# Kernel optimization log

Hardware: AMD Instinct MI355X
Metric: run time of the kernel (lower is better)

Reference implementation:

```python
import jax, jax.numpy as jnp
import numpy as np

# Qwen3-MoE style config
B, S, D = 2, 2048, 2048        # batch, seqlen, hidden_size
E, I, TOPK = 64, 768, 8        # num_experts, moe_intermediate_size, num_experts_per_tok
M = B * S                      # tokens
CAP = 2 * (M * TOPK) // E


def setup_inputs() -> dict:
    key = jax.random.key(0)
    k0, k1, k2, k3, k4 = jax.random.split(key, 5)
    return {
        "x": jax.random.normal(k0, (B, S, D), jnp.float32),
        "router_weight": jax.random.normal(k1, (D, E), jnp.float32) * 0.02,
        "gate_proj": jax.random.normal(k2, (E, D, I), jnp.float32) * 0.02,
        "up_proj": jax.random.normal(k3, (E, D, I), jnp.float32) * 0.02,
        "down_proj": jax.random.normal(k4, (E, I, D), jnp.float32) * 0.02,
    }


def _moe(x, router_weight, gate_proj, up_proj, down_proj):
    b, s, d = x.shape
    xf = x.reshape(-1, d)                                  # [M, d]
    m = xf.shape[0]

    # ---- TokenChoiceTopKRouter: softmax scores, top-k, renormalize ----
    logits = xf @ router_weight                            # [M, E]
    probs = jax.nn.softmax(logits.astype(jnp.float32), axis=-1)
    topw, topi = jax.lax.top_k(probs, TOPK)                # [M, k]
    topw = topw / topw.sum(axis=-1, keepdims=True)         # norm_topk_prob

    flat_e = topi.reshape(-1)                              # [M*k] expert id per assignment
    flat_w = topw.reshape(-1).astype(x.dtype)              # [M*k] routing weight per assignment

    # ---- permute: sort assignments by expert (stable) ----
    order = jnp.argsort(flat_e)                            # [M*k]
    se = flat_e[order]                                     # sorted expert ids
    tok = order // TOPK                                    # source token per sorted assignment
    counts = jax.ops.segment_sum(jnp.ones_like(flat_e), flat_e, num_segments=E)
    starts = jnp.cumsum(counts) - counts                   # exclusive prefix sum
    pos = jnp.arange(m * TOPK) - starts[se]                # slot within expert's buffer
    valid = pos < CAP
    posc = jnp.minimum(pos, CAP - 1)

    # ---- dispatch to padded per-expert buffers [E, CAP, d] ----
    xe = jnp.zeros((E, CAP, d), x.dtype).at[se, pos].set(xf[tok], mode='drop')

    # ---- grouped SwiGLU experts (batched GEMMs) ----
    h = jax.nn.silu(jnp.einsum('ecd,edi->eci', xe, gate_proj)) \
        * jnp.einsum('ecd,edi->eci', xe, up_proj)          # [E, CAP, I]
    ye = jnp.einsum('eci,eid->ecd', h, down_proj)          # [E, CAP, d]

    # ---- unpermute + weighted combine ----
    contrib = jnp.where(valid[:, None], ye[se, posc], 0.0) * flat_w[order][:, None]
    out = jnp.zeros((m, d), x.dtype).at[tok].add(contrib)  # sum over topk per token
    return out.reshape(b, s, d)


def reference(x, router_weight, gate_proj, up_proj, down_proj):
    return _moe(x, router_weight, gate_proj, up_proj, down_proj)
```

## Files before the change

### kernel.cpp

```cpp
#include <hip/hip_runtime.h>
#include <hip/hip_bf16.h>

typedef __attribute__((ext_vector_type(4))) float f32x4;
typedef __attribute__((ext_vector_type(8))) short bf16x8;
typedef __attribute__((ext_vector_type(8))) unsigned short us8;
typedef unsigned int   u32;
typedef unsigned short u16;

#define D_DIM 2048
#define I_DIM 768
#define NE    64
#define CAP   1024
#define NTOK  4096

__device__ __forceinline__ u32 cvt2(float a, float b) {
  __hip_bfloat162 hh = __float22bfloat162_rn(float2{a, b});
  union { __hip_bfloat162 h; u32 u; } c; c.h = hh; return c.u;
}
__device__ __forceinline__ u16 f2b(float f) {
  __hip_bfloat16 b = __float2bfloat16(f);
  union { __hip_bfloat16 b; u16 u; } c; c.b = b; return c.u;
}
__device__ __forceinline__ float b2f(u16 v) {
  union { u32 u; float f; } c; c.u = (u32)v << 16; return c.f;
}
__device__ __forceinline__ void glp16(const void* g, void* l) {
  __builtin_amdgcn_global_load_lds(
      (const __attribute__((address_space(1))) u32*)g,
      (__attribute__((address_space(3))) u32*)l, 16, 0, 0);
}

#define VMW(n) asm volatile("s_waitcnt vmcnt(" #n ")" ::: "memory")
#define BARF   do { __builtin_amdgcn_s_barrier(); \
                    asm volatile("" ::: "memory"); } while (0)

__global__ __launch_bounds__(256) void k_cvt_x(const float* __restrict__ x,
                                               u16* __restrict__ xb) {
  const size_t i = ((size_t)blockIdx.x * 256 + threadIdx.x) * 8;
  float4 v0 = *(const float4*)(x + i);
  float4 v1 = *(const float4*)(x + i + 4);
  uint4 o;
  o.x = cvt2(v0.x, v0.y); o.y = cvt2(v0.z, v0.w);
  o.z = cvt2(v1.x, v1.y); o.w = cvt2(v1.z, v1.w);
  *(uint4*)(xb + i) = o;
}

__global__ __launch_bounds__(256) void k_router(
    const float* __restrict__ x, const float* __restrict__ rw,
    int* __restrict__ counts, int* __restrict__ slot_token,
    float* __restrict__ slot_w)
{
  const int lane = threadIdx.x & 63;
  const int tok  = blockIdx.x * 4 + (threadIdx.x >> 6);
  const float* xr = x + (size_t)tok * D_DIM;

  float acc = 0.f;
  for (int d0 = 0; d0 < D_DIM; d0 += 64) {
    float xv = xr[d0 + lane];
    #pragma unroll
    for (int j = 0; j < 64; ++j) {
      float xj = __shfl(xv, j, 64);
      acc = fmaf(xj, rw[(size_t)(d0 + j) * NE + lane], acc);
    }
  }

  float v = acc; int vi = lane;
  float wk[8]; int ei[8];
  float mx0 = 0.f, wsum = 0.f;
  #pragma unroll
  for (int k = 0; k < 8; ++k) {
    float mv = v; int mi = vi;
    #pragma unroll
    for (int off = 32; off >= 1; off >>= 1) {
      float ov = __shfl_xor(mv, off, 64);
      int   oi = __shfl_xor(mi, off, 64);
      if (ov > mv || (ov == mv && oi < mi)) { mv = ov; mi = oi; }
    }
    if (k == 0) mx0 = mv;
    float ew = __expf(mv - mx0);
    wk[k] = ew; ei[k] = mi; wsum += ew;
    if (lane == mi) v = -3.4e38f;
  }

  if (lane == 0) {
    float inv = 1.f / wsum;
    #pragma unroll
    for (int k = 0; k < 8; ++k) {
      int ee   = ei[k];
      int slot = atomicAdd(&counts[ee], 1);
      if (slot < CAP) {
        slot_token[ee * CAP + slot] = tok;
        slot_w[ee * CAP + slot]     = wk[k] * inv;
      }
    }
  }
}

__global__ __launch_bounds__(256) void k_inv(
    const int* __restrict__ counts, const int* __restrict__ slot_token,
    int* __restrict__ tok_cnt, int* __restrict__ tok_idx)
{
  const int e = blockIdx.x;
  int cnt = counts[e]; if (cnt > CAP) cnt = CAP;
  for (int s = threadIdx.x; s < cnt; s += 256) {
    const int tok = slot_token[e * CAP + s];
    const int pos = atomicAdd(&tok_cnt[tok], 1);
    if (pos < 8) tok_idx[tok * 8 + pos] = e * CAP + s;
  }
}

__global__ __launch_bounds__(256) void k_wpack(const float* __restrict__ in,
                                               u16* __restrict__ outp,
                                               int R, int C) {
  const int e  = blockIdx.z;
  const int c0 = blockIdx.x * 64;
  const int r0 = blockIdx.y * 64;
  const float* ip = in + (size_t)e * R * C;
  u16* op = outp + (size_t)e * (size_t)(C / 64) * (R / 8) * 512
                 + ((size_t)(c0 / 64) * (R / 8) + (r0 / 8)) * 512;

  __shared__ u16 T[64][76];
  const int t  = threadIdx.x;
  const int rr = t >> 4;
  const int cc = (t & 15) * 4;
  #pragma unroll
  for (int it = 0; it < 4; ++it) {
    const int r = rr + it * 16;
    float4 v = *(const float4*)(ip + (size_t)(r0 + r) * C + c0 + cc);
    T[cc + 0][r] = f2b(v.x);
    T[cc + 1][r] = f2b(v.y);
    T[cc + 2][r] = f2b(v.z);
    T[cc + 3][r] = f2b(v.w);
  }
  __syncthreads();
  const int n = t & 63;
  #pragma unroll
  for (int p = 0; p < 2; ++p) {
    const int c = (t >> 6) + p * 4;
    const u16* s = &T[n][c * 8];
    uint4 o;
    o.x = (u32)s[0] | ((u32)s[1] << 16);
    o.y = (u32)s[2] | ((u32)s[3] << 16);
    o.z = (u32)s[4] | ((u32)s[5] << 16);
    o.w = (u32)s[6] | ((u32)s[7] << 16);
    *(uint4*)(op + ((size_t)c * 64 + n) * 8) = o;
  }
}

__global__ __launch_bounds__(256) void k_xpack(
    const u16* __restrict__ xb, const int* __restrict__ counts,
    const int* __restrict__ slot_token, u16* __restrict__ xeT)
{
  const int e   = blockIdx.z;
  const int s0  = blockIdx.y * 64;
  const int kc0 = blockIdx.x * 32;
  int cnt = counts[e]; if (cnt > CAP) cnt = CAP;

  __shared__ u16 T[64][264];
  const int t = threadIdx.x;
  const int r = t >> 2;
  const int q = t & 3;
  const int  tok  = slot_token[e * CAP + s0 + r];
  const bool live = (s0 + r) < cnt;
  const u16* src = xb + (size_t)tok * D_DIM + kc0 * 8;

  #pragma unroll
  for (int it = 0; it < 8; ++it) {
    const int kl = it * 32 + q * 8;
    us8 v = {0, 0, 0, 0, 0, 0, 0, 0};
    if (live) v = *(const us8*)(src + kl);
    *(us8*)&T[r][kl] = v;
  }
  __syncthreads();

  u16* dst = xeT + (size_t)e * 2097152 + (size_t)kc0 * 8192 + (size_t)s0 * 8;
  const int sl = t & 63;
  #pragma unroll
  for (int p = 0; p < 8; ++p) {
    const int c = (t >> 6) + p * 4;
    const u16* s = &T[sl][c * 8];
    uint4 o = *(const uint4*)s;
    *(uint4*)(dst + (size_t)c * 8192 + sl * 8) = o;
  }
}


__device__ __forceinline__ void m1_issue(
    const u16* xeA, const u16* gbp, const u16* ubp, u16* sm,
    int js, int sb, int wv, int lane, int m0)
{
  const int st = sb * 16384;
  if (wv < 4) {
    const u16* s = xeA + (size_t)(js * 4) * 8192 + (size_t)(m0 + wv * 64 + lane) * 8;
    u16* d = sm + st + (wv * 64) * 8;
    glp16(s,         d);
    glp16(s + 8192,  d + 2048);
    glp16(s + 16384, d + 4096);
    glp16(s + 24576, d + 6144);
  } else {
    const int w2 = wv & 1;
    const u16* base = (wv >= 6) ? ubp : gbp;
    const u16* s = base + (size_t)w2 * 131072 + (size_t)(js * 4) * 512 + lane * 8;
    u16* d = sm + st + ((wv >= 6) ? 12288 : 8192) + (w2 * 64) * 8;
    glp16(s,        d);
    glp16(s + 512,  d + 1024);
    glp16(s + 1024, d + 2048);
    glp16(s + 1536, d + 3072);
  }
}

__device__ __forceinline__ void m1_step(
    const u16* sm, int st, int gq, int li, int mrow, int icol,
    f32x4 (&ag)[4][4], f32x4 (&au)[4][4])
{
  bf16x8 a[4], g[4], u[4];
  #pragma unroll
  for (int mf = 0; mf < 4; ++mf)
    a[mf] = *(const bf16x8*)&sm[st + (gq * 256 + mrow + mf * 16 + li) * 8];
  #pragma unroll
  for (int nf = 0; nf < 4; ++nf) {
    g[nf] = *(const bf16x8*)&sm[st + 8192  + (gq * 128 + icol + nf * 16 + li) * 8];
    u[nf] = *(const bf16x8*)&sm[st + 12288 + (gq * 128 + icol + nf * 16 + li) * 8];
  }
  #pragma unroll
  for (int mf = 0; mf < 4; ++mf)
    #pragma unroll
    for (int nf = 0; nf < 4; ++nf) {
      ag[mf][nf] = __builtin_amdgcn_mfma_f32_16x16x32_bf16(a[mf], g[nf], ag[mf][nf], 0, 0, 0);
      au[mf][nf] = __builtin_amdgcn_mfma_f32_16x16x32_bf16(a[mf], u[nf], au[mf][nf], 0, 0, 0);
    }
}

__global__ __launch_bounds__(512, 2) void k_mlp1p(
    const u16* __restrict__ xeT, const u16* __restrict__ Gpk,
    const u16* __restrict__ Upk, const int* __restrict__ counts,
    u16* __restrict__ hP)
{
  extern __shared__ u16 sm[];
  const int i   = blockIdx.x;
  const int xcd = i & 7;
  const int p   = i >> 3;
  const int mt  = p & 3;
  const int pe  = p >> 2;
  const int val = pe * 8 + xcd;
  const int e   = val / 6;
  const int nt  = val % 6;

  int cnt = counts[e]; if (cnt > CAP) cnt = CAP;
  const int m0 = mt * 256;
  if (m0 >= cnt) return;

  const int t = threadIdx.x;
  const int lane = t & 63, wv = t >> 6;
  const int li = lane & 15, gq = lane >> 4;
  const int mrow = (wv >> 1) * 64, icol = (wv & 1) * 64;

  const u16* xeA = xeT + (size_t)e * 2097152;
  const u16* gbp = Gpk + (size_t)e * 1572864 + (size_t)(nt * 2) * 131072;
  const u16* ubp = Upk + (size_t)e * 1572864 + (size_t)(nt * 2) * 131072;

  f32x4 ag[4][4], au[4][4];
  #pragma unroll
  for (int mf = 0; mf < 4; ++mf)
    #pragma unroll
    for (int nf = 0; nf < 4; ++nf) {
      f32x4 z = {0.f, 0.f, 0.f, 0.f};
      ag[mf][nf] = z; au[mf][nf] = z;
    }

  m1_issue(xeA, gbp, ubp, sm, 0, 0, wv, lane, m0);
  m1_issue(xeA, gbp, ubp, sm, 1, 1, wv, lane, m0);
  m1_issue(xeA, gbp, ubp, sm, 2, 2, wv, lane, m0);

  for (int j = 0; j < 61; ++j) {
    VMW(8); BARF;
    m1_issue(xeA, gbp, ubp, sm, j + 3, (j + 3) & 3, wv, lane, m0);
    m1_step(sm, (j & 3) * 16384, gq, li, mrow, icol, ag, au);
  }
  VMW(8); BARF; m1_step(sm, 1 * 16384, gq, li, mrow, icol, ag, au);
  VMW(4); BARF; m1_step(sm, 2 * 16384, gq, li, mrow, icol, ag, au);
  VMW(0); BARF; m1_step(sm, 3 * 16384, gq, li, mrow, icol, ag, au);

  u16* hPe = hP + (size_t)e * 786432;
  #pragma unroll
  for (int mf = 0; mf < 4; ++mf)
    #pragma unroll
    for (int jj = 0; jj < 4; ++jj) {
      const int slot = m0 + mrow + mf * 16 + gq * 4 + jj;
      #pragma unroll
      for (int nf = 0; nf < 4; ++nf) {
        const int ii = nt * 128 + icol + nf * 16 + li;
        float gg = ag[mf][nf][jj];
        float uu = au[mf][nf][jj];
        hPe[(size_t)(ii >> 3) * 8192 + slot * 8 + (ii & 7)] =
            f2b(gg * uu / (1.f + __expf(-gg)));
      }
    }
}

__device__ __forceinline__ void m2_issue(
    const u16* hPe, const u16* dpe, u16* sm,
    int js, int sb, int wv, int lane, int m0)
{
  const int st = sb * 16384;
  if (wv < 4) {
    const u16* s = hPe + (size_t)(js * 4) * 8192 + (size_t)(m0 + wv * 64 + lane) * 8;
    u16* d = sm + st + (wv * 64) * 8;
    glp16(s,         d);
    glp16(s + 8192,  d + 2048);
    glp16(s + 16384, d + 4096);
    glp16(s + 24576, d + 6144);
  } else {
    const int w2 = wv - 4;
    const u16* s = dpe + (size_t)w2 * 49152 + (size_t)(js * 4) * 512 + lane * 8;
    u16* d = sm + st + 8192 + (w2 * 64) * 8;
    glp16(s,        d);
    glp16(s + 512,  d + 2048);
    glp16(s + 1024, d + 4096);
    glp16(s + 1536, d + 6144);
  }
}

__device__ __forceinline__ void m2_step(
    const u16* sm, int st, int gq, int li, int mrow, int ncol,
    f32x4 (&acc)[4][8])
{
  bf16x8 a[4], b[8];
  #pragma unroll
  for (int mf = 0; mf < 4; ++mf)
    a[mf] = *(const bf16x8*)&sm[st + (gq * 256 + mrow + mf * 16 + li) * 8];
  #pragma unroll
  for (int nf = 0; nf < 8; ++nf)
    b[nf] = *(const bf16x8*)&sm[st + 8192 + (gq * 256 + ncol + nf * 16 + li) * 8];
  #pragma unroll
  for (int mf = 0; mf < 4; ++mf)
    #pragma unroll
    for (int nf = 0; nf < 8; ++nf)
      acc[mf][nf] = __builtin_amdgcn_mfma_f32_16x16x32_bf16(a[mf], b[nf], acc[mf][nf], 0, 0, 0);
}

__global__ __launch_bounds__(512, 2) void k_mlp2p(
    const u16* __restrict__ hP, const u16* __restrict__ Dpk,
    const int* __restrict__ counts, const float* __restrict__ slot_w,
    u16* __restrict__ ye)
{
  extern __shared__ u16 sm[];
  const int i   = blockIdx.x;
  const int xcd = i & 7;
  const int p   = i >> 3;
  const int mt  = p & 3;
  const int pe  = p >> 2;
  const int val = pe * 8 + xcd;
  const int e   = val >> 3;
  const int nt  = val & 7;

  int cnt = counts[e]; if (cnt > CAP) cnt = CAP;
  const int m0 = mt * 256;
  if (m0 >= cnt) return;
  const int n0 = nt * 256;

  const int t = threadIdx.x;
  const int lane = t & 63, wv = t >> 6;
  const int li = lane & 15, gq = lane >> 4;
  const int mrow = (wv >> 1) * 64, ncol = (wv & 1) * 128;

  const u16* hPe = hP + (size_t)e * 786432;
  const u16* dpe = Dpk + (size_t)e * 1572864 + (size_t)(nt * 4) * 49152;

  f32x4 acc[4][8];
  #pragma unroll
  for (int mf = 0; mf < 4; ++mf)
    #pragma unroll
    for (int nf = 0; nf < 8; ++nf) { f32x4 z = {0.f,0.f,0.f,0.f}; acc[mf][nf] = z; }

  m2_issue(hPe, dpe, sm, 0, 0, wv, lane, m0);
  m2_issue(hPe, dpe, sm, 1, 1, wv, lane, m0);
  m2_issue(hPe, dpe, sm, 2, 2, wv, lane, m0);

  for (int j = 0; j < 21; ++j) {
    VMW(8); BARF;
    m2_issue(hPe, dpe, sm, j + 3, (j + 3) & 3, wv, lane, m0);
    m2_step(sm, (j & 3) * 16384, gq, li, mrow, ncol, acc);
  }
  VMW(8); BARF; m2_step(sm, 1 * 16384, gq, li, mrow, ncol, acc);
  VMW(4); BARF; m2_step(sm, 2 * 16384, gq, li, mrow, ncol, acc);
  VMW(0); BARF; m2_step(sm, 3 * 16384, gq, li, mrow, ncol, acc);

  #pragma unroll
  for (int mf = 0; mf < 4; ++mf)
    #pragma unroll
    for (int jj = 0; jj < 4; ++jj) {
      const int slot = m0 + mrow + mf * 16 + gq * 4 + jj;
      if (slot < cnt) {
        const float wgt = slot_w[e * CAP + slot];
        u16* yr = ye + (size_t)(e * CAP + slot) * D_DIM + n0 + ncol + li;
        #pragma unroll
        for (int nf = 0; nf < 8; ++nf)
          yr[nf * 16] = f2b(wgt * acc[mf][nf][jj]);
      }
    }
}

__global__ __launch_bounds__(256) void k_combine(
    const u16* __restrict__ ye, const int* __restrict__ tok_idx,
    const int* __restrict__ tok_cnt, float* __restrict__ out)
{
  const int tok = blockIdx.x;
  const int c0  = threadIdx.x * 8;
  int cnt8 = tok_cnt[tok]; if (cnt8 > 8) cnt8 = 8;

  float s[8] = {0.f, 0.f, 0.f, 0.f, 0.f, 0.f, 0.f, 0.f};
  #pragma unroll
  for (int k = 0; k < 8; ++k) {
    if (k < cnt8) {
      const int idx = tok_idx[tok * 8 + k];
      const us8 v = *(const us8*)(ye + (size_t)idx * D_DIM + c0);
      #pragma unroll
      for (int j = 0; j < 8; ++j) s[j] += b2f(v[j]);
    }
  }
  float4 o0 = {s[0], s[1], s[2], s[3]};
  float4 o1 = {s[4], s[5], s[6], s[7]};
  float* op = out + (size_t)tok * D_DIM + c0;
  *(float4*)op       = o0;
  *(float4*)(op + 4) = o1;
}

extern "C" void kernel_launch(void* const* d_in, const int* in_sizes, int n_in,
                              void* d_out, int out_size, void* d_ws, size_t ws_size,
                              hipStream_t stream) {
  const float* x    = (const float*)d_in[0];
  const float* rw   = (const float*)d_in[1];
  const float* gate = (const float*)d_in[2];
  const float* up   = (const float*)d_in[3];
  const float* down = (const float*)d_in[4];
  float* out = (float*)d_out;

  char* ws = (char*)d_ws;
  int*   counts     = (int*)ws;
  int*   slot_token = (int*)(ws + 1024);
  float* slot_w     = (float*)(ws + 263168);
  u16*   xb         = (u16*)(ws + 525312);
  u16*   hP         = (u16*)(ws + 17302528);
  u16*   Gpk        = (u16*)(ws + 117965824);
  u16*   Upk        = (u16*)(ws + 319292416);
  u16*   xeT        = (u16*)(ws + 520619008);
  u16*   Dpk        = xeT;
  u16*   ye         = Gpk;
  int*   tok_cnt    = (int*)(ws + 721945600);
  int*   tok_idx    = (int*)(ws + 721945600 + 16384);

  hipFuncSetAttribute((const void*)k_mlp1p,
                      hipFuncAttributeMaxDynamicSharedMemorySize, 131072);
  hipFuncSetAttribute((const void*)k_mlp2p,
                      hipFuncAttributeMaxDynamicSharedMemorySize, 131072);

  hipMemsetAsync(counts, 0, NE * sizeof(int), stream);
  hipMemsetAsync(slot_token, 0, (size_t)NE * CAP * sizeof(int), stream);

  k_cvt_x <<<dim3((NTOK * D_DIM) / (256 * 8)), 256, 0, stream>>>(x, xb);
  k_router<<<dim3(NTOK / 4),                   256, 0, stream>>>(x, rw, counts, slot_token, slot_w);

  k_wpack<<<dim3(12, 32, NE), 256, 0, stream>>>(gate, Gpk, D_DIM, I_DIM);
  k_wpack<<<dim3(12, 32, NE), 256, 0, stream>>>(up,   Upk, D_DIM, I_DIM);
  k_xpack<<<dim3(8, 16, NE),  256, 0, stream>>>(xb, counts, slot_token, xeT);
  k_mlp1p<<<dim3(1536), 512, 131072, stream>>>(xeT, Gpk, Upk, counts, hP);

  hipMemsetAsync(tok_cnt, 0, NTOK * sizeof(int), stream);
  k_inv  <<<dim3(NE), 256, 0, stream>>>(counts, slot_token, tok_cnt, tok_idx);
  k_wpack<<<dim3(32, 12, NE), 256, 0, stream>>>(down, Dpk, I_DIM, D_DIM);

  k_mlp2p  <<<dim3(2048), 512, 131072, stream>>>(hP, Dpk, counts, slot_w, ye);
  k_combine<<<dim3(NTOK), 256, 0, stream>>>(ye, tok_idx, tok_cnt, out);
}
```

Before: 1.249 ms.

## Make expert GEMM blocks loop over all live M-tiles with continuous prefetch pipeline

Each workgroup in both expert GEMM kernels now owns one (expert, N-tile) pair and walks every live 256-row M tile of that expert in sequence. The global-to-LDS prefetch pipeline runs straight across tile boundaries, with an epilogue and accumulator reset at each tile end. This removes the per-block pipeline warm-up and drain and the launch of idle blocks for empty M tiles. The cost is far fewer workgroups (384 and 512 instead of 1536 and 2048), which risks lower occupancy and load imbalance, since experts with more tokens run longer.

```diff
diff --git a/kernel.cpp b/kernel.cpp
--- a/kernel.cpp
+++ b/kernel.cpp
@@ -187,11 +187,11 @@
 
 __device__ __forceinline__ void m1_issue(
     const u16* xeA, const u16* gbp, const u16* ubp, u16* sm,
-    int js, int sb, int wv, int lane, int m0)
+    int js, int sb, int wv, int lane, int sm0)
 {
   const int st = sb * 16384;
   if (wv < 4) {
-    const u16* s = xeA + (size_t)(js * 4) * 8192 + (size_t)(m0 + wv * 64 + lane) * 8;
+    const u16* s = xeA + (size_t)(js * 4) * 8192 + (size_t)(sm0 + wv * 64 + lane) * 8;
     u16* d = sm + st + (wv * 64) * 8;
     glp16(s,         d);
     glp16(s + 8192,  d + 2048);
@@ -231,57 +231,10 @@
     }
 }
 
-__global__ __launch_bounds__(512, 2) void k_mlp1p(
-    const u16* __restrict__ xeT, const u16* __restrict__ Gpk,
-    const u16* __restrict__ Upk, const int* __restrict__ counts,
-    u16* __restrict__ hP)
-{
-  extern __shared__ u16 sm[];
-  const int i   = blockIdx.x;
-  const int xcd = i & 7;
-  const int p   = i >> 3;
-  const int mt  = p & 3;
-  const int pe  = p >> 2;
-  const int val = pe * 8 + xcd;
-  const int e   = val / 6;
-  const int nt  = val % 6;
-
-  int cnt = counts[e]; if (cnt > CAP) cnt = CAP;
-  const int m0 = mt * 256;
-  if (m0 >= cnt) return;
-
-  const int t = threadIdx.x;
-  const int lane = t & 63, wv = t >> 6;
-  const int li = lane & 15, gq = lane >> 4;
-  const int mrow = (wv >> 1) * 64, icol = (wv & 1) * 64;
-
-  const u16* xeA = xeT + (size_t)e * 2097152;
-  const u16* gbp = Gpk + (size_t)e * 1572864 + (size_t)(nt * 2) * 131072;
-  const u16* ubp = Upk + (size_t)e * 1572864 + (size_t)(nt * 2) * 131072;
-
-  f32x4 ag[4][4], au[4][4];
-  #pragma unroll
-  for (int mf = 0; mf < 4; ++mf)
-    #pragma unroll
-    for (int nf = 0; nf < 4; ++nf) {
-      f32x4 z = {0.f, 0.f, 0.f, 0.f};
-      ag[mf][nf] = z; au[mf][nf] = z;
-    }
-
-  m1_issue(xeA, gbp, ubp, sm, 0, 0, wv, lane, m0);
-  m1_issue(xeA, gbp, ubp, sm, 1, 1, wv, lane, m0);
-  m1_issue(xeA, gbp, ubp, sm, 2, 2, wv, lane, m0);
-
-  for (int j = 0; j < 61; ++j) {
-    VMW(8); BARF;
-    m1_issue(xeA, gbp, ubp, sm, j + 3, (j + 3) & 3, wv, lane, m0);
-    m1_step(sm, (j & 3) * 16384, gq, li, mrow, icol, ag, au);
-  }
-  VMW(8); BARF; m1_step(sm, 1 * 16384, gq, li, mrow, icol, ag, au);
-  VMW(4); BARF; m1_step(sm, 2 * 16384, gq, li, mrow, icol, ag, au);
-  VMW(0); BARF; m1_step(sm, 3 * 16384, gq, li, mrow, icol, ag, au);
-
-  u16* hPe = hP + (size_t)e * 786432;
+__device__ __forceinline__ void m1_epi(
+    u16* hPe, int nt, int m0, int mrow, int icol, int gq, int li,
+    f32x4 (&ag)[4][4], f32x4 (&au)[4][4])
+{
   #pragma unroll
   for (int mf = 0; mf < 4; ++mf)
     #pragma unroll
@@ -296,15 +249,80 @@
             f2b(gg * uu / (1.f + __expf(-gg)));
       }
     }
+  #pragma unroll
+  for (int mf = 0; mf < 4; ++mf)
+    #pragma unroll
+    for (int nf = 0; nf < 4; ++nf) {
+      f32x4 z = {0.f, 0.f, 0.f, 0.f};
+      ag[mf][nf] = z; au[mf][nf] = z;
+    }
+}
+
+__global__ __launch_bounds__(512, 2) void k_mlp1p(
+    const u16* __restrict__ xeT, const u16* __restrict__ Gpk,
+    const u16* __restrict__ Upk, const int* __restrict__ counts,
+    u16* __restrict__ hP)
+{
+  extern __shared__ u16 sm[];
+  const int i   = blockIdx.x;
+  const int xcd = i & 7;
+  const int p   = i >> 3;
+  const int val = p * 8 + xcd;
+  const int e   = val / 6;
+  const int nt  = val % 6;
+
+  int cnt = counts[e]; if (cnt > CAP) cnt = CAP;
+  if (cnt <= 0) return;
+  const int nlive = (cnt + 255) >> 8;
+  const int NT = nlive * 64;
+
+  const int t = threadIdx.x;
+  const int lane = t & 63, wv = t >> 6;
+  const int li = lane & 15, gq = lane >> 4;
+  const int mrow = (wv >> 1) * 64, icol = (wv & 1) * 64;
+
+  const u16* xeA = xeT + (size_t)e * 2097152;
+  const u16* gbp = Gpk + (size_t)e * 1572864 + (size_t)(nt * 2) * 131072;
+  const u16* ubp = Upk + (size_t)e * 1572864 + (size_t)(nt * 2) * 131072;
+  u16* hPe = hP + (size_t)e * 786432;
+
+  f32x4 ag[4][4], au[4][4];
+  #pragma unroll
+  for (int mf = 0; mf < 4; ++mf)
+    #pragma unroll
+    for (int nf = 0; nf < 4; ++nf) {
+      f32x4 z = {0.f, 0.f, 0.f, 0.f};
+      ag[mf][nf] = z; au[mf][nf] = z;
+    }
+
+  m1_issue(xeA, gbp, ubp, sm, 0, 0, wv, lane, 0);
+  m1_issue(xeA, gbp, ubp, sm, 1, 1, wv, lane, 0);
+  m1_issue(xeA, gbp, ubp, sm, 2, 2, wv, lane, 0);
+
+  for (int jj = 0; jj < NT - 3; ++jj) {
+    VMW(8); BARF;
+    const int s = jj + 3;
+    m1_issue(xeA, gbp, ubp, sm, s & 63, s & 3, wv, lane, (s >> 6) * 256);
+    m1_step(sm, (jj & 3) * 16384, gq, li, mrow, icol, ag, au);
+    if ((jj & 63) == 63)
+      m1_epi(hPe, nt, (jj >> 6) * 256, mrow, icol, gq, li, ag, au);
+  }
+  { const int jj = NT - 3; VMW(8); BARF;
+    m1_step(sm, (jj & 3) * 16384, gq, li, mrow, icol, ag, au); }
+  { const int jj = NT - 2; VMW(4); BARF;
+    m1_step(sm, (jj & 3) * 16384, gq, li, mrow, icol, ag, au); }
+  { const int jj = NT - 1; VMW(0); BARF;
+    m1_step(sm, (jj & 3) * 16384, gq, li, mrow, icol, ag, au);
+    m1_epi(hPe, nt, (jj >> 6) * 256, mrow, icol, gq, li, ag, au); }
 }
 
 __device__ __forceinline__ void m2_issue(
     const u16* hPe, const u16* dpe, u16* sm,
-    int js, int sb, int wv, int lane, int m0)
+    int ph, int sb, int wv, int lane, int sm0)
 {
   const int st = sb * 16384;
   if (wv < 4) {
-    const u16* s = hPe + (size_t)(js * 4) * 8192 + (size_t)(m0 + wv * 64 + lane) * 8;
+    const u16* s = hPe + (size_t)(ph * 4) * 8192 + (size_t)(sm0 + wv * 64 + lane) * 8;
     u16* d = sm + st + (wv * 64) * 8;
     glp16(s,         d);
     glp16(s + 8192,  d + 2048);
@@ -312,7 +330,7 @@
     glp16(s + 24576, d + 6144);
   } else {
     const int w2 = wv - 4;
-    const u16* s = dpe + (size_t)w2 * 49152 + (size_t)(js * 4) * 512 + lane * 8;
+    const u16* s = dpe + (size_t)w2 * 49152 + (size_t)(ph * 4) * 512 + lane * 8;
     u16* d = sm + st + 8192 + (w2 * 64) * 8;
     glp16(s,        d);
     glp16(s + 512,  d + 2048);
@@ -339,6 +357,29 @@
       acc[mf][nf] = __builtin_amdgcn_mfma_f32_16x16x32_bf16(a[mf], b[nf], acc[mf][nf], 0, 0, 0);
 }
 
+__device__ __forceinline__ void m2_epi(
+    u16* ye, int cnt, const float* slot_w, int eCAP, int n0, int m0,
+    int mrow, int ncol, int gq, int li, f32x4 (&acc)[4][8])
+{
+  #pragma unroll
+  for (int mf = 0; mf < 4; ++mf)
+    #pragma unroll
+    for (int jj = 0; jj < 4; ++jj) {
+      const int slot = m0 + mrow + mf * 16 + gq * 4 + jj;
+      if (slot < cnt) {
+        const float wgt = slot_w[eCAP + slot];
+        u16* yr = ye + (size_t)(eCAP + slot) * D_DIM + n0 + ncol + li;
+        #pragma unroll
+        for (int nf = 0; nf < 8; ++nf)
+          yr[nf * 16] = f2b(wgt * acc[mf][nf][jj]);
+      }
+    }
+  #pragma unroll
+  for (int mf = 0; mf < 4; ++mf)
+    #pragma unroll
+    for (int nf = 0; nf < 8; ++nf) { f32x4 z = {0.f,0.f,0.f,0.f}; acc[mf][nf] = z; }
+}
+
 __global__ __launch_bounds__(512, 2) void k_mlp2p(
     const u16* __restrict__ hP, const u16* __restrict__ Dpk,
     const int* __restrict__ counts, const float* __restrict__ slot_w,
@@ -348,15 +389,14 @@
   const int i   = blockIdx.x;
   const int xcd = i & 7;
   const int p   = i >> 3;
-  const int mt  = p & 3;
-  const int pe  = p >> 2;
-  const int val = pe * 8 + xcd;
+  const int val = p * 8 + xcd;
   const int e   = val >> 3;
   const int nt  = val & 7;
 
   int cnt = counts[e]; if (cnt > CAP) cnt = CAP;
-  const int m0 = mt * 256;
-  if (m0 >= cnt) return;
+  if (cnt <= 0) return;
+  const int nlive = (cnt + 255) >> 8;
+  const int NT = nlive * 24;
   const int n0 = nt * 256;
 
   const int t = threadIdx.x;
@@ -366,6 +406,7 @@
 
   const u16* hPe = hP + (size_t)e * 786432;
   const u16* dpe = Dpk + (size_t)e * 1572864 + (size_t)(nt * 4) * 49152;
+  const int eCAP = e * CAP;
 
   f32x4 acc[4][8];
   #pragma unroll
@@ -373,32 +414,27 @@
     #pragma unroll
     for (int nf = 0; nf < 8; ++nf) { f32x4 z = {0.f,0.f,0.f,0.f}; acc[mf][nf] = z; }
 
-  m2_issue(hPe, dpe, sm, 0, 0, wv, lane, m0);
-  m2_issue(hPe, dpe, sm, 1, 1, wv, lane, m0);
-  m2_issue(hPe, dpe, sm, 2, 2, wv, lane, m0);
-
-  for (int j = 0; j < 21; ++j) {
+  m2_issue(hPe, dpe, sm, 0, 0, wv, lane, 0);
+  m2_issue(hPe, dpe, sm, 1, 1, wv, lane, 0);
+  m2_issue(hPe, dpe, sm, 2, 2, wv, lane, 0);
+
+  for (int jj = 0; jj < NT - 3; ++jj) {
     VMW(8); BARF;
-    m2_issue(hPe, dpe, sm, j + 3, (j + 3) & 3, wv, lane, m0);
-    m2_step(sm, (j & 3) * 16384, gq, li, mrow, ncol, acc);
-  }
-  VMW(8); BARF; m2_step(sm, 1 * 16384, gq, li, mrow, ncol, acc);
-  VMW(4); BARF; m2_step(sm, 2 * 16384, gq, li, mrow, ncol, acc);
-  VMW(0); BARF; m2_step(sm, 3 * 16384, gq, li, mrow, ncol, acc);
-
-  #pragma unroll
-  for (int mf = 0; mf < 4; ++mf)
-    #pragma unroll
-    for (int jj = 0; jj < 4; ++jj) {
-      const int slot = m0 + mrow + mf * 16 + gq * 4 + jj;
-      if (slot < cnt) {
-        const float wgt = slot_w[e * CAP + slot];
-        u16* yr = ye + (size_t)(e * CAP + slot) * D_DIM + n0 + ncol + li;
-        #pragma unroll
-        for (int nf = 0; nf < 8; ++nf)
-          yr[nf * 16] = f2b(wgt * acc[mf][nf][jj]);
-      }
-    }
+    const int s    = jj + 3;
+    const int tixs = (s >= 72) ? 3 : (s >= 48) ? 2 : (s >= 24) ? 1 : 0;
+    m2_issue(hPe, dpe, sm, s - tixs * 24, s & 3, wv, lane, tixs * 256);
+    m2_step(sm, (jj & 3) * 16384, gq, li, mrow, ncol, acc);
+    const int tixj = (jj >= 72) ? 3 : (jj >= 48) ? 2 : (jj >= 24) ? 1 : 0;
+    if (jj - tixj * 24 == 23)
+      m2_epi(ye, cnt, slot_w, eCAP, n0, tixj * 256, mrow, ncol, gq, li, acc);
+  }
+  { const int jj = NT - 3; VMW(8); BARF;
+    m2_step(sm, (jj & 3) * 16384, gq, li, mrow, ncol, acc); }
+  { const int jj = NT - 2; VMW(4); BARF;
+    m2_step(sm, (jj & 3) * 16384, gq, li, mrow, ncol, acc); }
+  { const int jj = NT - 1; VMW(0); BARF;
+    m2_step(sm, (jj & 3) * 16384, gq, li, mrow, ncol, acc);
+    m2_epi(ye, cnt, slot_w, eCAP, n0, (nlive - 1) * 256, mrow, ncol, gq, li, acc); }
 }
 
 __global__ __launch_bounds__(256) void k_combine(
@@ -464,12 +500,12 @@
   k_wpack<<<dim3(12, 32, NE), 256, 0, stream>>>(gate, Gpk, D_DIM, I_DIM);
   k_wpack<<<dim3(12, 32, NE), 256, 0, stream>>>(up,   Upk, D_DIM, I_DIM);
   k_xpack<<<dim3(8, 16, NE),  256, 0, stream>>>(xb, counts, slot_token, xeT);
-  k_mlp1p<<<dim3(1536), 512, 131072, stream>>>(xeT, Gpk, Upk, counts, hP);
+  k_mlp1p<<<dim3(384), 512, 131072, stream>>>(xeT, Gpk, Upk, counts, hP);
 
   hipMemsetAsync(tok_cnt, 0, NTOK * sizeof(int), stream);
   k_inv  <<<dim3(NE), 256, 0, stream>>>(counts, slot_token, tok_cnt, tok_idx);
   k_wpack<<<dim3(32, 12, NE), 256, 0, stream>>>(down, Dpk, I_DIM, D_DIM);
 
-  k_mlp2p  <<<dim3(2048), 512, 131072, stream>>>(hP, Dpk, counts, slot_w, ye);
+  k_mlp2p  <<<dim3(512), 512, 131072, stream>>>(hP, Dpk, counts, slot_w, ye);
   k_combine<<<dim3(NTOK), 256, 0, stream>>>(ye, tok_idx, tok_cnt, out);
 }
```

Measured after the change: 1.310 ms. +4.9%, slower.

## Halve grouped-GEMM M tile to 128 with 256-thread blocks and triple-buffered LDS

Applied to the files above, without the earlier changes.

Both expert GEMM kernels move from 256-row tiles with 512 threads and a 4-stage LDS ring to 128-row tiles with 256 threads and a 3-stage ring. Each block now uses 72 KB of shared memory instead of 128 KB, and the grids double. The load-issue code is rewritten so 4 waves cover A and B tile loads. The aim is finer granularity, so experts with fewer tokens waste less padded work and more blocks fit per CU. In exchange, the B weight tiles are read twice as often per expert, and the pipeline is one stage shallower.

```diff
diff --git a/kernel.cpp b/kernel.cpp
--- a/kernel.cpp
+++ b/kernel.cpp
@@ -186,41 +186,40 @@
 
 
 __device__ __forceinline__ void m1_issue(
-    const u16* xeA, const u16* gbp, const u16* ubp, u16* sm,
-    int js, int sb, int wv, int lane, int m0)
-{
-  const int st = sb * 16384;
-  if (wv < 4) {
-    const u16* s = xeA + (size_t)(js * 4) * 8192 + (size_t)(m0 + wv * 64 + lane) * 8;
-    u16* d = sm + st + (wv * 64) * 8;
-    glp16(s,         d);
-    glp16(s + 8192,  d + 2048);
-    glp16(s + 16384, d + 4096);
-    glp16(s + 24576, d + 6144);
-  } else {
-    const int w2 = wv & 1;
-    const u16* base = (wv >= 6) ? ubp : gbp;
-    const u16* s = base + (size_t)w2 * 131072 + (size_t)(js * 4) * 512 + lane * 8;
-    u16* d = sm + st + ((wv >= 6) ? 12288 : 8192) + (w2 * 64) * 8;
-    glp16(s,        d);
-    glp16(s + 512,  d + 1024);
-    glp16(s + 1024, d + 2048);
-    glp16(s + 1536, d + 3072);
+    const u16* xeA, const u16* gb, const u16* ub, u16* st,
+    int js, int wv, int lane, int m0)
+{
+  #pragma unroll
+  for (int q = 0; q < 6; ++q) {
+    const int id = wv * 6 + q;
+    const int kc = (id >> 1) & 3;
+    const int h  = id & 1;
+    const size_t kcA = (size_t)(js * 4 + kc);
+    if (id < 8) {
+      glp16(xeA + kcA * 8192 + (size_t)(m0 + h * 64 + lane) * 8,
+            st + kc * 1024 + h * 512);
+    } else if (id < 16) {
+      glp16(gb + (size_t)h * 131072 + kcA * 512 + lane * 8,
+            st + 4096 + kc * 1024 + h * 512);
+    } else {
+      glp16(ub + (size_t)h * 131072 + kcA * 512 + lane * 8,
+            st + 8192 + kc * 1024 + h * 512);
+    }
   }
 }
 
 __device__ __forceinline__ void m1_step(
-    const u16* sm, int st, int gq, int li, int mrow, int icol,
+    const u16* st, int gq, int li, int mrow, int icol,
     f32x4 (&ag)[4][4], f32x4 (&au)[4][4])
 {
   bf16x8 a[4], g[4], u[4];
   #pragma unroll
   for (int mf = 0; mf < 4; ++mf)
-    a[mf] = *(const bf16x8*)&sm[st + (gq * 256 + mrow + mf * 16 + li) * 8];
+    a[mf] = *(const bf16x8*)&st[(gq * 128 + mrow + mf * 16 + li) * 8];
   #pragma unroll
   for (int nf = 0; nf < 4; ++nf) {
-    g[nf] = *(const bf16x8*)&sm[st + 8192  + (gq * 128 + icol + nf * 16 + li) * 8];
-    u[nf] = *(const bf16x8*)&sm[st + 12288 + (gq * 128 + icol + nf * 16 + li) * 8];
+    g[nf] = *(const bf16x8*)&st[4096 + (gq * 128 + icol + nf * 16 + li) * 8];
+    u[nf] = *(const bf16x8*)&st[8192 + (gq * 128 + icol + nf * 16 + li) * 8];
   }
   #pragma unroll
   for (int mf = 0; mf < 4; ++mf)
@@ -231,7 +230,7 @@
     }
 }
 
-__global__ __launch_bounds__(512, 2) void k_mlp1p(
+__global__ __launch_bounds__(256, 2) void k_mlp1p(
     const u16* __restrict__ xeT, const u16* __restrict__ Gpk,
     const u16* __restrict__ Upk, const int* __restrict__ counts,
     u16* __restrict__ hP)
@@ -240,14 +239,14 @@
   const int i   = blockIdx.x;
   const int xcd = i & 7;
   const int p   = i >> 3;
-  const int mt  = p & 3;
-  const int pe  = p >> 2;
+  const int mt  = p & 7;
+  const int pe  = p >> 3;
   const int val = pe * 8 + xcd;
   const int e   = val / 6;
   const int nt  = val % 6;
 
   int cnt = counts[e]; if (cnt > CAP) cnt = CAP;
-  const int m0 = mt * 256;
+  const int m0 = mt * 128;
   if (m0 >= cnt) return;
 
   const int t = threadIdx.x;
@@ -256,8 +255,9 @@
   const int mrow = (wv >> 1) * 64, icol = (wv & 1) * 64;
 
   const u16* xeA = xeT + (size_t)e * 2097152;
-  const u16* gbp = Gpk + (size_t)e * 1572864 + (size_t)(nt * 2) * 131072;
-  const u16* ubp = Upk + (size_t)e * 1572864 + (size_t)(nt * 2) * 131072;
+  const u16* gb  = Gpk + (size_t)e * 1572864 + (size_t)(nt * 2) * 131072;
+  const u16* ub  = Upk + (size_t)e * 1572864 + (size_t)(nt * 2) * 131072;
+  u16* hPe = hP + (size_t)e * 786432;
 
   f32x4 ag[4][4], au[4][4];
   #pragma unroll
@@ -268,20 +268,17 @@
       ag[mf][nf] = z; au[mf][nf] = z;
     }
 
-  m1_issue(xeA, gbp, ubp, sm, 0, 0, wv, lane, m0);
-  m1_issue(xeA, gbp, ubp, sm, 1, 1, wv, lane, m0);
-  m1_issue(xeA, gbp, ubp, sm, 2, 2, wv, lane, m0);
-
-  for (int j = 0; j < 61; ++j) {
-    VMW(8); BARF;
-    m1_issue(xeA, gbp, ubp, sm, j + 3, (j + 3) & 3, wv, lane, m0);
-    m1_step(sm, (j & 3) * 16384, gq, li, mrow, icol, ag, au);
-  }
-  VMW(8); BARF; m1_step(sm, 1 * 16384, gq, li, mrow, icol, ag, au);
-  VMW(4); BARF; m1_step(sm, 2 * 16384, gq, li, mrow, icol, ag, au);
-  VMW(0); BARF; m1_step(sm, 3 * 16384, gq, li, mrow, icol, ag, au);
-
-  u16* hPe = hP + (size_t)e * 786432;
+  m1_issue(xeA, gb, ub, sm,         0, wv, lane, m0);
+  m1_issue(xeA, gb, ub, sm + 12288, 1, wv, lane, m0);
+
+  for (int j = 0; j < 62; ++j) {
+    VMW(6); BARF;
+    m1_issue(xeA, gb, ub, sm + ((j + 2) % 3) * 12288, j + 2, wv, lane, m0);
+    m1_step(sm + (j % 3) * 12288, gq, li, mrow, icol, ag, au);
+  }
+  VMW(6); BARF; m1_step(sm + 2 * 12288, gq, li, mrow, icol, ag, au);
+  VMW(0); BARF; m1_step(sm + 0 * 12288, gq, li, mrow, icol, ag, au);
+
   #pragma unroll
   for (int mf = 0; mf < 4; ++mf)
     #pragma unroll
@@ -299,39 +296,39 @@
 }
 
 __device__ __forceinline__ void m2_issue(
-    const u16* hPe, const u16* dpe, u16* sm,
-    int js, int sb, int wv, int lane, int m0)
-{
-  const int st = sb * 16384;
-  if (wv < 4) {
-    const u16* s = hPe + (size_t)(js * 4) * 8192 + (size_t)(m0 + wv * 64 + lane) * 8;
-    u16* d = sm + st + (wv * 64) * 8;
-    glp16(s,         d);
-    glp16(s + 8192,  d + 2048);
-    glp16(s + 16384, d + 4096);
-    glp16(s + 24576, d + 6144);
-  } else {
-    const int w2 = wv - 4;
-    const u16* s = dpe + (size_t)w2 * 49152 + (size_t)(js * 4) * 512 + lane * 8;
-    u16* d = sm + st + 8192 + (w2 * 64) * 8;
-    glp16(s,        d);
-    glp16(s + 512,  d + 2048);
-    glp16(s + 1024, d + 4096);
-    glp16(s + 1536, d + 6144);
+    const u16* hPe, const u16* dp, u16* st,
+    int js, int wv, int lane, int m0)
+{
+  #pragma unroll
+  for (int q = 0; q < 6; ++q) {
+    const int id = wv * 6 + q;
+    const size_t kcA = (size_t)(js * 4 + ((id < 8) ? ((id >> 1) & 3) : ((id - 8) & 3)));
+    if (id < 8) {
+      const int kc = (id >> 1) & 3;
+      const int h  = id & 1;
+      glp16(hPe + kcA * 8192 + (size_t)(m0 + h * 64 + lane) * 8,
+            st + kc * 1024 + h * 512);
+    } else {
+      const int r  = id - 8;
+      const int kc = r & 3;
+      const int ng = r >> 2;
+      glp16(dp + (size_t)ng * 49152 + kcA * 512 + lane * 8,
+            st + 4096 + kc * 2048 + ng * 512);
+    }
   }
 }
 
 __device__ __forceinline__ void m2_step(
-    const u16* sm, int st, int gq, int li, int mrow, int ncol,
+    const u16* st, int gq, int li, int mrow, int ncol,
     f32x4 (&acc)[4][8])
 {
   bf16x8 a[4], b[8];
   #pragma unroll
   for (int mf = 0; mf < 4; ++mf)
-    a[mf] = *(const bf16x8*)&sm[st + (gq * 256 + mrow + mf * 16 + li) * 8];
+    a[mf] = *(const bf16x8*)&st[(gq * 128 + mrow + mf * 16 + li) * 8];
   #pragma unroll
   for (int nf = 0; nf < 8; ++nf)
-    b[nf] = *(const bf16x8*)&sm[st + 8192 + (gq * 256 + ncol + nf * 16 + li) * 8];
+    b[nf] = *(const bf16x8*)&st[4096 + (gq * 256 + ncol + nf * 16 + li) * 8];
   #pragma unroll
   for (int mf = 0; mf < 4; ++mf)
     #pragma unroll
@@ -339,7 +336,7 @@
       acc[mf][nf] = __builtin_amdgcn_mfma_f32_16x16x32_bf16(a[mf], b[nf], acc[mf][nf], 0, 0, 0);
 }
 
-__global__ __launch_bounds__(512, 2) void k_mlp2p(
+__global__ __launch_bounds__(256, 2) void k_mlp2p(
     const u16* __restrict__ hP, const u16* __restrict__ Dpk,
     const int* __restrict__ counts, const float* __restrict__ slot_w,
     u16* __restrict__ ye)
@@ -348,14 +345,14 @@
   const int i   = blockIdx.x;
   const int xcd = i & 7;
   const int p   = i >> 3;
-  const int mt  = p & 3;
-  const int pe  = p >> 2;
+  const int mt  = p & 7;
+  const int pe  = p >> 3;
   const int val = pe * 8 + xcd;
   const int e   = val >> 3;
   const int nt  = val & 7;
 
   int cnt = counts[e]; if (cnt > CAP) cnt = CAP;
-  const int m0 = mt * 256;
+  const int m0 = mt * 128;
   if (m0 >= cnt) return;
   const int n0 = nt * 256;
 
@@ -365,7 +362,8 @@
   const int mrow = (wv >> 1) * 64, ncol = (wv & 1) * 128;
 
   const u16* hPe = hP + (size_t)e * 786432;
-  const u16* dpe = Dpk + (size_t)e * 1572864 + (size_t)(nt * 4) * 49152;
+  const u16* dp  = Dpk + (size_t)e * 1572864 + (size_t)(nt * 4) * 49152;
+  const int eCAP = e * CAP;
 
   f32x4 acc[4][8];
   #pragma unroll
@@ -373,18 +371,16 @@
     #pragma unroll
     for (int nf = 0; nf < 8; ++nf) { f32x4 z = {0.f,0.f,0.f,0.f}; acc[mf][nf] = z; }
 
-  m2_issue(hPe, dpe, sm, 0, 0, wv, lane, m0);
-  m2_issue(hPe, dpe, sm, 1, 1, wv, lane, m0);
-  m2_issue(hPe, dpe, sm, 2, 2, wv, lane, m0);
-
-  for (int j = 0; j < 21; ++j) {
-    VMW(8); BARF;
-    m2_issue(hPe, dpe, sm, j + 3, (j + 3) & 3, wv, lane, m0);
-    m2_step(sm, (j & 3) * 16384, gq, li, mrow, ncol, acc);
-  }
-  VMW(8); BARF; m2_step(sm, 1 * 16384, gq, li, mrow, ncol, acc);
-  VMW(4); BARF; m2_step(sm, 2 * 16384, gq, li, mrow, ncol, acc);
-  VMW(0); BARF; m2_step(sm, 3 * 16384, gq, li, mrow, ncol, acc);
+  m2_issue(hPe, dp, sm,         0, wv, lane, m0);
+  m2_issue(hPe, dp, sm + 12288, 1, wv, lane, m0);
+
+  for (int j = 0; j < 22; ++j) {
+    VMW(6); BARF;
+    m2_issue(hPe, dp, sm + ((j + 2) % 3) * 12288, j + 2, wv, lane, m0);
+    m2_step(sm + (j % 3) * 12288, gq, li, mrow, ncol, acc);
+  }
+  VMW(6); BARF; m2_step(sm + (22 % 3) * 12288, gq, li, mrow, ncol, acc);
+  VMW(0); BARF; m2_step(sm + (23 % 3) * 12288, gq, li, mrow, ncol, acc);
 
   #pragma unroll
   for (int mf = 0; mf < 4; ++mf)
@@ -392,8 +388,8 @@
     for (int jj = 0; jj < 4; ++jj) {
       const int slot = m0 + mrow + mf * 16 + gq * 4 + jj;
       if (slot < cnt) {
-        const float wgt = slot_w[e * CAP + slot];
-        u16* yr = ye + (size_t)(e * CAP + slot) * D_DIM + n0 + ncol + li;
+        const float wgt = slot_w[eCAP + slot];
+        u16* yr = ye + (size_t)(eCAP + slot) * D_DIM + n0 + ncol + li;
         #pragma unroll
         for (int nf = 0; nf < 8; ++nf)
           yr[nf * 16] = f2b(wgt * acc[mf][nf][jj]);
@@ -451,9 +447,9 @@
   int*   tok_idx    = (int*)(ws + 721945600 + 16384);
 
   hipFuncSetAttribute((const void*)k_mlp1p,
-                      hipFuncAttributeMaxDynamicSharedMemorySize, 131072);
+                      hipFuncAttributeMaxDynamicSharedMemorySize, 73728);
   hipFuncSetAttribute((const void*)k_mlp2p,
-                      hipFuncAttributeMaxDynamicSharedMemorySize, 131072);
+                      hipFuncAttributeMaxDynamicSharedMemorySize, 73728);
 
   hipMemsetAsync(counts, 0, NE * sizeof(int), stream);
   hipMemsetAsync(slot_token, 0, (size_t)NE * CAP * sizeof(int), stream);
@@ -464,12 +460,12 @@
   k_wpack<<<dim3(12, 32, NE), 256, 0, stream>>>(gate, Gpk, D_DIM, I_DIM);
   k_wpack<<<dim3(12, 32, NE), 256, 0, stream>>>(up,   Upk, D_DIM, I_DIM);
   k_xpack<<<dim3(8, 16, NE),  256, 0, stream>>>(xb, counts, slot_token, xeT);
-  k_mlp1p<<<dim3(1536), 512, 131072, stream>>>(xeT, Gpk, Upk, counts, hP);
+  k_mlp1p<<<dim3(3072), 256, 73728, stream>>>(xeT, Gpk, Upk, counts, hP);
 
   hipMemsetAsync(tok_cnt, 0, NTOK * sizeof(int), stream);
   k_inv  <<<dim3(NE), 256, 0, stream>>>(counts, slot_token, tok_cnt, tok_idx);
   k_wpack<<<dim3(32, 12, NE), 256, 0, stream>>>(down, Dpk, I_DIM, D_DIM);
 
-  k_mlp2p  <<<dim3(2048), 512, 131072, stream>>>(hP, Dpk, counts, slot_w, ye);
+  k_mlp2p  <<<dim3(4096), 256, 73728, stream>>>(hP, Dpk, counts, slot_w, ye);
   k_combine<<<dim3(NTOK), 256, 0, stream>>>(ye, tok_idx, tok_cnt, out);
 }
```

New measurement: 1.190 ms. -4.8%, faster.
